# Optimization experiments

Measured on AMD Instinct MI355X. Metric: run time of the kernel, lower is better.

## Reference

```python
import jax, jax.numpy as jnp
import numpy as np

N = 400000          # total component rows
M = 100000          # number of mixtures (segments)
EMB = 128           # component_emb_dim
CTX = 256           # context_dim
LAT = 256           # latent_dim


def setup_inputs() -> dict:
    key = jax.random.key(0)
    ks = jax.random.split(key, 12)
    comp_emb = jax.random.normal(ks[0], (N, EMB), dtype=jnp.float32)
    mole_frac = jax.random.uniform(ks[1], (N,), dtype=jnp.float32)
    component_batch_batch = jax.random.randint(ks[2], (N,), 0, M, dtype=jnp.int32)
    s = 0.05
    # interaction_mlp: Linear(EMB+1, CTX) -> Softplus -> Linear(CTX, CTX) -> Softplus
    iW1 = jax.random.normal(ks[3], (EMB + 1, CTX), dtype=jnp.float32) * s
    ib1 = jnp.zeros((CTX,), dtype=jnp.float32)
    iW2 = jax.random.normal(ks[4], (CTX, CTX), dtype=jnp.float32) * s
    ib2 = jnp.zeros((CTX,), dtype=jnp.float32)
    # gate_mlp: Linear(EMB+1+CTX, LAT) -> Softplus -> Linear(LAT, LAT) -> Softplus
    gW1 = jax.random.normal(ks[5], (EMB + 1 + CTX, LAT), dtype=jnp.float32) * s
    gb1 = jnp.zeros((LAT,), dtype=jnp.float32)
    gW2 = jax.random.normal(ks[6], (LAT, LAT), dtype=jnp.float32) * s
    gb2 = jnp.zeros((LAT,), dtype=jnp.float32)
    return {
        "comp_emb": comp_emb, "mole_frac": mole_frac,
        "component_batch_batch": component_batch_batch,
        "iW1": iW1, "ib1": ib1, "iW2": iW2, "ib2": ib2,
        "gW1": gW1, "gb1": gb1, "gW2": gW2, "gb2": gb2,
    }


def reference(comp_emb, mole_frac, component_batch_batch,
              iW1, ib1, iW2, ib2, gW1, gb1, gW2, gb2):
    seg = component_batch_batch
    # raw_context_input = cat([comp_emb, mole_frac[:, None]], -1)  -> [N, EMB+1]
    raw = jnp.concatenate([comp_emb, mole_frac[:, None]], axis=-1)
    # global_mean_pool: segment mean over mixtures -> [M, EMB+1]
    seg_sum = jax.ops.segment_sum(raw, seg, num_segments=M)
    counts = jax.ops.segment_sum(jnp.ones((raw.shape[0],), raw.dtype), seg,
                                 num_segments=M)
    pooled = seg_sum / jnp.maximum(counts, 1.0)[:, None]
    # interaction MLP on pooled context -> [M, CTX]
    h = jax.nn.softplus(pooled @ iW1 + ib1)
    ctx = jax.nn.softplus(h @ iW2 + ib2)
    # broadcast back to per-component rows -> [N, CTX]
    ctx_exp = ctx[seg]
    # gate MLP -> [N, LAT]
    gate_in = jnp.concatenate([comp_emb, mole_frac[:, None], ctx_exp], axis=-1)
    g = jax.nn.softplus(gate_in @ gW1 + gb1)
    latent = jax.nn.softplus(g @ gW2 + gb2)
    return (latent, mole_frac)
```

## Files before the change

### kernel.cpp

```cpp
#include <hip/hip_runtime.h>

#define N_ROWS 400000
#define M_SEG  100000
#define EMB    128
#define SSTR   132
#define AST    168
#define S1     5
#define S2     8

typedef _Float16 f16x8 __attribute__((ext_vector_type(8)));
typedef float    f32x4 __attribute__((ext_vector_type(4)));

__device__ __forceinline__ unsigned short h_bits(_Float16 h) {
    unsigned short u; __builtin_memcpy(&u, &h, 2); return u;
}
__device__ __forceinline__ float f_from_bits(unsigned short u) {
    _Float16 h; __builtin_memcpy(&h, &u, 2); return (float)h;
}
__device__ __forceinline__ float softplus_f(float x) {
    return fmaxf(x, 0.f) + __logf(1.f + __expf(-fabsf(x)));
}

#define KLOOP(STEPS, AIDX, BH)                                                      \
  for (int s = 0; s < (STEPS); ++s) {                                               \
    f16x8 ah[4], bhv[2];                                                            \
    _Pragma("unroll")                                                               \
    for (int mt = 0; mt < 4; ++mt) {                                                \
      const int ai = (AIDX);                                                        \
      ah[mt] = *reinterpret_cast<const f16x8*>(&lds[ai]);                           \
    }                                                                               \
    _Pragma("unroll")                                                               \
    for (int nt = 0; nt < 2; ++nt) {                                                \
      const size_t bo = (((size_t)s * 16 + w * 2 + nt) * 64 + lane) * 8;            \
      bhv[nt] = *reinterpret_cast<const f16x8*>(&(BH)[bo]);                         \
    }                                                                               \
    _Pragma("unroll")                                                               \
    for (int mt = 0; mt < 4; ++mt) {                                                \
      _Pragma("unroll")                                                             \
      for (int nt = 0; nt < 2; ++nt) {                                              \
        acc[mt][nt] = __builtin_amdgcn_mfma_f32_16x16x32_f16(ah[mt], bhv[nt], acc[mt][nt], 0, 0, 0); \
      }                                                                             \
    }                                                                               \
  }

#define WRITE_ACT_LDS()                                                   \
  _Pragma("unroll")                                                       \
  for (int mt = 0; mt < 4; ++mt)                                          \
    _Pragma("unroll")                                                     \
    for (int nt = 0; nt < 2; ++nt)                                        \
      _Pragma("unroll")                                                   \
      for (int r = 0; r < 4; ++r) {                                       \
        const float hv = softplus_f(acc[mt][nt][r]);                      \
        const int row = mt * 16 + 4 * g + r;                              \
        const int col = w * 32 + nt * 16 + cc;                            \
        const int si  = ((row * 256 + col) ^ ((row & 7) << 3));           \
        lds[si] = h_bits((_Float16)hv);                                   \
      }

#define ACC_INIT_BIAS(BPTR)                                   \
  _Pragma("unroll")                                           \
  for (int nt = 0; nt < 2; ++nt) {                            \
    const float b = (BPTR)[w * 32 + nt * 16 + cc];            \
    _Pragma("unroll")                                         \
    for (int mt = 0; mt < 4; ++mt)                            \
      _Pragma("unroll")                                       \
      for (int r = 0; r < 4; ++r) acc[mt][nt][r] = b;         \
  }

#define AIDX_L1 ((mt * 16 + cc) * AST + s * 32 + g * 8)
#define AIDX_SW ((((mt * 16 + cc) * 256 + s * 32 + g * 8)) ^ ((cc & 7) << 3))

__global__ __launch_bounds__(256) void count_kernel(
    const int* __restrict__ seg, int* __restrict__ cnt) {
    int i = blockIdx.x * 256 + threadIdx.x;
    if (i < N_ROWS) atomicAdd(&cnt[seg[i]], 1);
}

__global__ __launch_bounds__(256) void scan_kernel(
    const int* __restrict__ cnt, int* __restrict__ excl,
    int* __restrict__ partials, int M) {
    __shared__ int tsum[256];
    const int t = threadIdx.x;
    const int b0 = blockIdx.x * 1024;
    int v[4]; int s = 0;
    #pragma unroll
    for (int j = 0; j < 4; ++j) {
        int idx = b0 + t * 4 + j;
        int c = (idx < M) ? cnt[idx] : 0;
        v[j] = s; s += c;
    }
    tsum[t] = s;
    __syncthreads();
    for (int off = 1; off < 256; off <<= 1) {
        int x = (t >= off) ? tsum[t - off] : 0;
        __syncthreads();
        tsum[t] += x;
        __syncthreads();
    }
    int tbase = (t > 0) ? tsum[t - 1] : 0;
    if (t == 255 && partials) partials[blockIdx.x] = tsum[255];
    #pragma unroll
    for (int j = 0; j < 4; ++j) {
        int idx = b0 + t * 4 + j;
        if (idx < M) excl[idx] = tbase + v[j];
    }
}

__global__ __launch_bounds__(256) void add_offsets_kernel(
    int* __restrict__ excl, const int* __restrict__ pex, int M) {
    int i = blockIdx.x * 256 + threadIdx.x;
    if (i < M) excl[i] += pex[i >> 10];
}

__global__ __launch_bounds__(256) void scatter_kernel(
    const int* __restrict__ seg, const int* __restrict__ base,
    int* __restrict__ cursor, int* __restrict__ rowids) {
    int i = blockIdx.x * 256 + threadIdx.x;
    if (i < N_ROWS) {
        int s = seg[i];
        int p = atomicAdd(&cursor[s], 1);
        rowids[base[s] + p] = i;
    }
}

__global__ __launch_bounds__(256) void pool_kernel(
    const float* __restrict__ comp_emb, const float* __restrict__ mf,
    const int* __restrict__ rowids, const int* __restrict__ base,
    float* __restrict__ seg_sum, float* __restrict__ countsf) {
    const int wid  = (blockIdx.x * 256 + threadIdx.x) >> 6;
    const int lane = threadIdx.x & 63;
    if (wid >= M_SEG) return;
    const int b = base[wid];
    const int e = (wid == M_SEG - 1) ? N_ROWS : base[wid + 1];
    float a0 = 0.f, a1 = 0.f, amf = 0.f;
    for (int j = b; j < e; ++j) {
        const int row = rowids[j];
        const float2 v = *reinterpret_cast<const float2*>(
            &comp_emb[(size_t)row * EMB + lane * 2]);
        a0 += v.x; a1 += v.y;
        if (lane == 0) amf += mf[row];
    }
    *reinterpret_cast<float2*>(&seg_sum[(size_t)wid * SSTR + lane * 2]) =
        make_float2(a0, a1);
    if (lane == 0) {
        seg_sum[(size_t)wid * SSTR + EMB] = amf;
        countsf[wid] = (float)(e - b);
    }
}

__global__ __launch_bounds__(256) void pack_w_kernel(
    const float* __restrict__ W, int K, int steps,
    unsigned short* __restrict__ ph) {
    int idx = blockIdx.x * 256 + threadIdx.x;
    if (idx >= steps * 1024) return;
    int lane = idx & 63, t = idx >> 6, nt = t & 15, s = t >> 4;
    int c  = nt * 16 + (lane & 15);
    int k0 = s * 32 + (lane >> 4) * 8;
    unsigned short h[8];
    #pragma unroll
    for (int j = 0; j < 8; ++j) {
        int k = k0 + j;
        float v = (k < K) ? W[(size_t)k * 256 + c] : 0.f;
        h[j] = h_bits((_Float16)v);
    }
    __builtin_memcpy(&ph[(size_t)idx * 8], h, 16);
}

__global__ __launch_bounds__(512, 6) void mix_mfma_kernel(
    const float* __restrict__ seg_sum, const float* __restrict__ counts,
    const unsigned short* __restrict__ i1h, const float* __restrict__ ib1,
    const unsigned short* __restrict__ i2h, const float* __restrict__ ib2,
    const unsigned short* __restrict__ gzh, const float* __restrict__ gb1,
    unsigned short* __restrict__ zh) {
    __shared__ unsigned short lds[64 * 256];
    const int m0  = blockIdx.x * 64;
    const int tid = threadIdx.x;
    const int w = tid >> 6, lane = tid & 63, g = lane >> 4, cc = lane & 15;

    for (int i = tid; i < 64 * 42; i += 512) {
        int r = i / 42, c4 = i - r * 42;
        int m = m0 + r;
        float x0 = 0.f, x1 = 0.f, x2 = 0.f, x3 = 0.f;
        if (m < M_SEG && c4 <= 32) {
            float inv = 1.f / fmaxf(counts[m], 1.f);
            if (c4 < 32) {
                const float4 v = *reinterpret_cast<const float4*>(&seg_sum[(size_t)m * SSTR + c4 * 4]);
                x0 = v.x * inv; x1 = v.y * inv; x2 = v.z * inv; x3 = v.w * inv;
            } else {
                x0 = seg_sum[(size_t)m * SSTR + EMB] * inv;
            }
        }
        uint2 hv = make_uint2((unsigned)h_bits((_Float16)x0) | ((unsigned)h_bits((_Float16)x1) << 16),
                              (unsigned)h_bits((_Float16)x2) | ((unsigned)h_bits((_Float16)x3) << 16));
        *reinterpret_cast<uint2*>(&lds[r * AST + c4 * 4]) = hv;
    }
    __syncthreads();

    f32x4 acc[4][2];
    ACC_INIT_BIAS(ib1)
    KLOOP(S1, AIDX_L1, i1h)
    __syncthreads();
    WRITE_ACT_LDS()
    __syncthreads();
    ACC_INIT_BIAS(ib2)
    KLOOP(S2, AIDX_SW, i2h)
    __syncthreads();
    WRITE_ACT_LDS()
    __syncthreads();
    ACC_INIT_BIAS(gb1)
    KLOOP(S2, AIDX_SW, gzh)
    #pragma unroll
    for (int mt = 0; mt < 4; ++mt)
        #pragma unroll
        for (int nt = 0; nt < 2; ++nt)
            #pragma unroll
            for (int r = 0; r < 4; ++r) {
                int m = m0 + mt * 16 + 4 * g + r;
                if (m < M_SEG)
                    zh[(size_t)m * 256 + w * 32 + nt * 16 + cc] =
                        h_bits((_Float16)acc[mt][nt][r]);
            }
}

__global__ __launch_bounds__(512, 6) void gate_mfma_kernel(
    const float* __restrict__ comp_emb, const float* __restrict__ mf,
    const int* __restrict__ seg, const unsigned short* __restrict__ zh,
    const unsigned short* __restrict__ g1h, const unsigned short* __restrict__ g2h,
    const float* __restrict__ gb2, float* __restrict__ out) {
    __shared__ unsigned short lds[64 * 256];
    const int n0  = blockIdx.x * 64;
    const int tid = threadIdx.x;
    const int w = tid >> 6, lane = tid & 63, g = lane >> 4, cc = lane & 15;

    f32x4 acc[4][2];
    int rs[4][4];
    #pragma unroll
    for (int mt = 0; mt < 4; ++mt)
        #pragma unroll
        for (int r = 0; r < 4; ++r)
            rs[mt][r] = seg[n0 + mt * 16 + 4 * g + r];
    #pragma unroll
    for (int mt = 0; mt < 4; ++mt)
        #pragma unroll
        for (int nt = 0; nt < 2; ++nt)
            #pragma unroll
            for (int r = 0; r < 4; ++r)
                acc[mt][nt][r] = f_from_bits(
                    zh[(size_t)rs[mt][r] * 256 + w * 32 + nt * 16 + cc]);

    for (int i = tid; i < 64 * 42; i += 512) {
        int r = i / 42, c4 = i - r * 42;
        int row = n0 + r;
        float x0 = 0.f, x1 = 0.f, x2 = 0.f, x3 = 0.f;
        if (c4 < 32) {
            const float4 v = *reinterpret_cast<const float4*>(&comp_emb[(size_t)row * EMB + c4 * 4]);
            x0 = v.x; x1 = v.y; x2 = v.z; x3 = v.w;
        } else if (c4 == 32) {
            x0 = mf[row];
        }
        uint2 hv = make_uint2((unsigned)h_bits((_Float16)x0) | ((unsigned)h_bits((_Float16)x1) << 16),
                              (unsigned)h_bits((_Float16)x2) | ((unsigned)h_bits((_Float16)x3) << 16));
        *reinterpret_cast<uint2*>(&lds[r * AST + c4 * 4]) = hv;
    }
    __syncthreads();

    KLOOP(S1, AIDX_L1, g1h)
    __syncthreads();
    WRITE_ACT_LDS()
    __syncthreads();
    ACC_INIT_BIAS(gb2)
    KLOOP(S2, AIDX_SW, g2h)
    #pragma unroll
    for (int mt = 0; mt < 4; ++mt)
        #pragma unroll
        for (int nt = 0; nt < 2; ++nt)
            #pragma unroll
            for (int r = 0; r < 4; ++r)
                out[(size_t)(n0 + mt * 16 + 4 * g + r) * 256 + w * 32 + nt * 16 + cc] =
                    softplus_f(acc[mt][nt][r]);
}

__global__ __launch_bounds__(256) void mf_copy_kernel(
    const float* __restrict__ mf, float* __restrict__ out) {
    int i = blockIdx.x * 256 + threadIdx.x;
    if (i < N_ROWS) out[(size_t)N_ROWS * 256 + i] = mf[i];
}

extern "C" void kernel_launch(void* const* d_in, const int* in_sizes, int n_in,
                              void* d_out, int out_size, void* d_ws, size_t ws_size,
                              hipStream_t stream) {
    const float* comp_emb = (const float*)d_in[0];
    const float* mf       = (const float*)d_in[1];
    const int*   seg      = (const int*)d_in[2];
    const float* iW1      = (const float*)d_in[3];
    const float* ib1      = (const float*)d_in[4];
    const float* iW2      = (const float*)d_in[5];
    const float* ib2      = (const float*)d_in[6];
    const float* gW1      = (const float*)d_in[7];
    const float* gb1      = (const float*)d_in[8];
    const float* gW2      = (const float*)d_in[9];
    const float* gb2      = (const float*)d_in[10];
    float* out = (float*)d_out;

    float* seg_sum = (float*)d_ws;
    float* countsf = seg_sum + (size_t)M_SEG * SSTR;
    unsigned short* zh = (unsigned short*)(countsf + M_SEG);
    unsigned short* i1h = zh + (size_t)M_SEG * 256;
    unsigned short* i2h = i1h + 40960;
    unsigned short* g1h = i2h + 65536;
    unsigned short* gzh = g1h + 40960;
    unsigned short* g2h = gzh + 65536;
    int* counts_i = (int*)(g2h + 65536);
    int* cursor   = counts_i + M_SEG;
    int* excl     = cursor + M_SEG;
    int* rowids   = excl + M_SEG;
    int* partials    = rowids + N_ROWS;
    int* partials_ex = partials + 128;

    hipMemsetAsync(counts_i, 0, 2 * (size_t)M_SEG * sizeof(int), stream);

    pack_w_kernel<<<20, 256, 0, stream>>>(iW1, 129, S1, i1h);
    pack_w_kernel<<<32, 256, 0, stream>>>(iW2, 256, S2, i2h);
    pack_w_kernel<<<20, 256, 0, stream>>>(gW1, 129, S1, g1h);
    pack_w_kernel<<<32, 256, 0, stream>>>(gW1 + 129 * 256, 256, S2, gzh);
    pack_w_kernel<<<32, 256, 0, stream>>>(gW2, 256, S2, g2h);

    const int nb_rows = (N_ROWS + 255) / 256;
    const int nb_scan = (M_SEG + 1023) / 1024;
    count_kernel<<<nb_rows, 256, 0, stream>>>(seg, counts_i);
    scan_kernel<<<nb_scan, 256, 0, stream>>>(counts_i, excl, partials, M_SEG);
    scan_kernel<<<1, 256, 0, stream>>>(partials, partials_ex, nullptr, nb_scan);
    add_offsets_kernel<<<(M_SEG + 255) / 256, 256, 0, stream>>>(excl, partials_ex, M_SEG);
    scatter_kernel<<<nb_rows, 256, 0, stream>>>(seg, excl, cursor, rowids);
    pool_kernel<<<(M_SEG * 64 + 255) / 256, 256, 0, stream>>>(
        comp_emb, mf, rowids, excl, seg_sum, countsf);

    mix_mfma_kernel<<<(M_SEG + 63) / 64, 512, 0, stream>>>(
        seg_sum, countsf, i1h, ib1, i2h, ib2, gzh, gb1, zh);
    gate_mfma_kernel<<<N_ROWS / 64, 512, 0, stream>>>(
        comp_emb, mf, seg, zh, g1h, g2h, gb2, out);
    mf_copy_kernel<<<(N_ROWS + 255) / 256, 256, 0, stream>>>(mf, out);
}
```

Baseline: 1.013 ms.

## Fuse segment pooling into mix kernel, prefetch weights, fold mf copy into gate

The separate pool kernel is removed. Each wave of the mix MFMA kernel now gathers and averages its own 8 segments straight into LDS, so the fp32 seg_sum array is never written to or read back from global memory. The MFMA k-loop now double-buffers the packed weight fragments, loading the next step's B operands while the current step computes. The mole_frac output copy moves into the gate kernel, which saves a launch. The trade-off is that segment-length imbalance now serializes inside each wave of a heavy 512-thread block, and the latency-bound gather loop may leave fewer waves in flight to hide latency.

```diff
diff --git a/kernel.cpp b/kernel.cpp
--- a/kernel.cpp
+++ b/kernel.cpp
@@ -3,7 +3,6 @@
 #define N_ROWS 400000
 #define M_SEG  100000
 #define EMB    128
-#define SSTR   132
 #define AST    168
 #define S1     5
 #define S2     8
@@ -21,25 +20,32 @@
     return fmaxf(x, 0.f) + __logf(1.f + __expf(-fabsf(x)));
 }
 
-#define KLOOP(STEPS, AIDX, BH)                                                      \
-  for (int s = 0; s < (STEPS); ++s) {                                               \
-    f16x8 ah[4], bhv[2];                                                            \
+#define KLOOP_P(STEPS, AIDX, BH)                                                    \
+  {                                                                                 \
+    f16x8 bcur[2], bnxt[2];                                                         \
     _Pragma("unroll")                                                               \
-    for (int mt = 0; mt < 4; ++mt) {                                                \
-      const int ai = (AIDX);                                                        \
-      ah[mt] = *reinterpret_cast<const f16x8*>(&lds[ai]);                           \
-    }                                                                               \
+    for (int nt = 0; nt < 2; ++nt)                                                  \
+      bcur[nt] = *reinterpret_cast<const f16x8*>(&(BH)[((size_t)(w * 2 + nt) * 64 + lane) * 8]); \
     _Pragma("unroll")                                                               \
-    for (int nt = 0; nt < 2; ++nt) {                                                \
-      const size_t bo = (((size_t)s * 16 + w * 2 + nt) * 64 + lane) * 8;            \
-      bhv[nt] = *reinterpret_cast<const f16x8*>(&(BH)[bo]);                         \
-    }                                                                               \
-    _Pragma("unroll")                                                               \
-    for (int mt = 0; mt < 4; ++mt) {                                                \
+    for (int s = 0; s < (STEPS); ++s) {                                             \
+      if (s + 1 < (STEPS)) {                                                        \
+        _Pragma("unroll")                                                           \
+        for (int nt = 0; nt < 2; ++nt)                                              \
+          bnxt[nt] = *reinterpret_cast<const f16x8*>(                               \
+              &(BH)[(((size_t)(s + 1) * 16 + w * 2 + nt) * 64 + lane) * 8]);        \
+      }                                                                             \
+      f16x8 ah[4];                                                                  \
       _Pragma("unroll")                                                             \
-      for (int nt = 0; nt < 2; ++nt) {                                              \
-        acc[mt][nt] = __builtin_amdgcn_mfma_f32_16x16x32_f16(ah[mt], bhv[nt], acc[mt][nt], 0, 0, 0); \
+      for (int mt = 0; mt < 4; ++mt) {                                              \
+        const int ai = (AIDX);                                                      \
+        ah[mt] = *reinterpret_cast<const f16x8*>(&lds[ai]);                         \
       }                                                                             \
+      _Pragma("unroll")                                                             \
+      for (int mt = 0; mt < 4; ++mt)                                                \
+        _Pragma("unroll")                                                           \
+        for (int nt = 0; nt < 2; ++nt)                                              \
+          acc[mt][nt] = __builtin_amdgcn_mfma_f32_16x16x32_f16(ah[mt], bcur[nt], acc[mt][nt], 0, 0, 0); \
+      bcur[0] = bnxt[0]; bcur[1] = bnxt[1];                                         \
     }                                                                               \
   }
 
@@ -123,31 +129,6 @@
     }
 }
 
-__global__ __launch_bounds__(256) void pool_kernel(
-    const float* __restrict__ comp_emb, const float* __restrict__ mf,
-    const int* __restrict__ rowids, const int* __restrict__ base,
-    float* __restrict__ seg_sum, float* __restrict__ countsf) {
-    const int wid  = (blockIdx.x * 256 + threadIdx.x) >> 6;
-    const int lane = threadIdx.x & 63;
-    if (wid >= M_SEG) return;
-    const int b = base[wid];
-    const int e = (wid == M_SEG - 1) ? N_ROWS : base[wid + 1];
-    float a0 = 0.f, a1 = 0.f, amf = 0.f;
-    for (int j = b; j < e; ++j) {
-        const int row = rowids[j];
-        const float2 v = *reinterpret_cast<const float2*>(
-            &comp_emb[(size_t)row * EMB + lane * 2]);
-        a0 += v.x; a1 += v.y;
-        if (lane == 0) amf += mf[row];
-    }
-    *reinterpret_cast<float2*>(&seg_sum[(size_t)wid * SSTR + lane * 2]) =
-        make_float2(a0, a1);
-    if (lane == 0) {
-        seg_sum[(size_t)wid * SSTR + EMB] = amf;
-        countsf[wid] = (float)(e - b);
-    }
-}
-
 __global__ __launch_bounds__(256) void pack_w_kernel(
     const float* __restrict__ W, int K, int steps,
     unsigned short* __restrict__ ph) {
@@ -167,7 +148,8 @@
 }
 
 __global__ __launch_bounds__(512, 6) void mix_mfma_kernel(
-    const float* __restrict__ seg_sum, const float* __restrict__ counts,
+    const float* __restrict__ comp_emb, const float* __restrict__ mf,
+    const int* __restrict__ rowids, const int* __restrict__ excl,
     const unsigned short* __restrict__ i1h, const float* __restrict__ ib1,
     const unsigned short* __restrict__ i2h, const float* __restrict__ ib2,
     const unsigned short* __restrict__ gzh, const float* __restrict__ gb1,
@@ -177,38 +159,48 @@
     const int tid = threadIdx.x;
     const int w = tid >> 6, lane = tid & 63, g = lane >> 4, cc = lane & 15;
 
-    for (int i = tid; i < 64 * 42; i += 512) {
-        int r = i / 42, c4 = i - r * 42;
-        int m = m0 + r;
-        float x0 = 0.f, x1 = 0.f, x2 = 0.f, x3 = 0.f;
-        if (m < M_SEG && c4 <= 32) {
-            float inv = 1.f / fmaxf(counts[m], 1.f);
-            if (c4 < 32) {
-                const float4 v = *reinterpret_cast<const float4*>(&seg_sum[(size_t)m * SSTR + c4 * 4]);
-                x0 = v.x * inv; x1 = v.y * inv; x2 = v.z * inv; x3 = v.w * inv;
-            } else {
-                x0 = seg_sum[(size_t)m * SSTR + EMB] * inv;
-            }
+    for (int q = 0; q < 8; ++q) {
+        const int ml = w * 8 + q;
+        const int m  = m0 + ml;
+        int b = 0, e = 0;
+        if (m < M_SEG) {
+            b = excl[m];
+            e = (m == M_SEG - 1) ? N_ROWS : excl[m + 1];
         }
-        uint2 hv = make_uint2((unsigned)h_bits((_Float16)x0) | ((unsigned)h_bits((_Float16)x1) << 16),
-                              (unsigned)h_bits((_Float16)x2) | ((unsigned)h_bits((_Float16)x3) << 16));
-        *reinterpret_cast<uint2*>(&lds[r * AST + c4 * 4]) = hv;
+        float a0 = 0.f, a1 = 0.f, amf = 0.f;
+        for (int j = b; j < e; ++j) {
+            const int row = rowids[j];
+            const float2 v = *reinterpret_cast<const float2*>(
+                &comp_emb[(size_t)row * EMB + lane * 2]);
+            a0 += v.x; a1 += v.y;
+            if (lane == 0) amf += mf[row];
+        }
+        const float inv = 1.f / fmaxf((float)(e - b), 1.f);
+        unsigned u = (unsigned)h_bits((_Float16)(a0 * inv)) |
+                     ((unsigned)h_bits((_Float16)(a1 * inv)) << 16);
+        *reinterpret_cast<unsigned*>(&lds[ml * AST + lane * 2]) = u;
+        if (lane == 0) {
+            unsigned um = (unsigned)h_bits((_Float16)(amf * inv));
+            *reinterpret_cast<unsigned*>(&lds[ml * AST + 128]) = um;
+        } else if (lane <= 15) {
+            *reinterpret_cast<unsigned*>(&lds[ml * AST + 128 + lane * 2]) = 0u;
+        }
     }
     __syncthreads();
 
     f32x4 acc[4][2];
     ACC_INIT_BIAS(ib1)
-    KLOOP(S1, AIDX_L1, i1h)
+    KLOOP_P(S1, AIDX_L1, i1h)
     __syncthreads();
     WRITE_ACT_LDS()
     __syncthreads();
     ACC_INIT_BIAS(ib2)
-    KLOOP(S2, AIDX_SW, i2h)
+    KLOOP_P(S2, AIDX_SW, i2h)
     __syncthreads();
     WRITE_ACT_LDS()
     __syncthreads();
     ACC_INIT_BIAS(gb1)
-    KLOOP(S2, AIDX_SW, gzh)
+    KLOOP_P(S2, AIDX_SW, gzh)
     #pragma unroll
     for (int mt = 0; mt < 4; ++mt)
         #pragma unroll
@@ -247,6 +239,10 @@
             for (int r = 0; r < 4; ++r)
                 acc[mt][nt][r] = f_from_bits(
                     zh[(size_t)rs[mt][r] * 256 + w * 32 + nt * 16 + cc]);
+
+    if (tid < 64) {
+        out[(size_t)N_ROWS * 256 + n0 + tid] = mf[n0 + tid];
+    }
 
     for (int i = tid; i < 64 * 42; i += 512) {
         int r = i / 42, c4 = i - r * 42;
@@ -264,12 +260,12 @@
     }
     __syncthreads();
 
-    KLOOP(S1, AIDX_L1, g1h)
+    KLOOP_P(S1, AIDX_L1, g1h)
     __syncthreads();
     WRITE_ACT_LDS()
     __syncthreads();
     ACC_INIT_BIAS(gb2)
-    KLOOP(S2, AIDX_SW, g2h)
+    KLOOP_P(S2, AIDX_SW, g2h)
     #pragma unroll
     for (int mt = 0; mt < 4; ++mt)
         #pragma unroll
@@ -278,12 +274,6 @@
             for (int r = 0; r < 4; ++r)
                 out[(size_t)(n0 + mt * 16 + 4 * g + r) * 256 + w * 32 + nt * 16 + cc] =
                     softplus_f(acc[mt][nt][r]);
-}
-
-__global__ __launch_bounds__(256) void mf_copy_kernel(
-    const float* __restrict__ mf, float* __restrict__ out) {
-    int i = blockIdx.x * 256 + threadIdx.x;
-    if (i < N_ROWS) out[(size_t)N_ROWS * 256 + i] = mf[i];
 }
 
 extern "C" void kernel_launch(void* const* d_in, const int* in_sizes, int n_in,
@@ -302,9 +292,7 @@
     const float* gb2      = (const float*)d_in[10];
     float* out = (float*)d_out;
 
-    float* seg_sum = (float*)d_ws;
-    float* countsf = seg_sum + (size_t)M_SEG * SSTR;
-    unsigned short* zh = (unsigned short*)(countsf + M_SEG);
+    unsigned short* zh  = (unsigned short*)d_ws;
     unsigned short* i1h = zh + (size_t)M_SEG * 256;
     unsigned short* i2h = i1h + 40960;
     unsigned short* g1h = i2h + 65536;
@@ -332,12 +320,9 @@
     scan_kernel<<<1, 256, 0, stream>>>(partials, partials_ex, nullptr, nb_scan);
     add_offsets_kernel<<<(M_SEG + 255) / 256, 256, 0, stream>>>(excl, partials_ex, M_SEG);
     scatter_kernel<<<nb_rows, 256, 0, stream>>>(seg, excl, cursor, rowids);
-    pool_kernel<<<(M_SEG * 64 + 255) / 256, 256, 0, stream>>>(
-        comp_emb, mf, rowids, excl, seg_sum, countsf);
 
     mix_mfma_kernel<<<(M_SEG + 63) / 64, 512, 0, stream>>>(
-        seg_sum, countsf, i1h, ib1, i2h, ib2, gzh, gb1, zh);
+        comp_emb, mf, rowids, excl, i1h, ib1, i2h, ib2, gzh, gb1, zh);
     gate_mfma_kernel<<<N_ROWS / 64, 512, 0, stream>>>(
         comp_emb, mf, seg, zh, g1h, g2h, gb2, out);
-    mf_copy_kernel<<<(N_ROWS + 255) / 256, 256, 0, stream>>>(mf, out);
-}
+}
```

Measured after the change: 997.1 us. About the same (-1.5%).
